# Performance work log

Hardware: AMD Instinct MI355X
Metric: run time of the kernel (lower is better)

Reference implementation:

```python
import jax, jax.numpy as jnp
import numpy as np

R_MAX = 32
S_MAX = 2
C_Z = 128
NTB = 2 * R_MAX + 2 + 1  # num_tok_pos_bins = 67
IN_DIM = 2 * NTB + (2 * S_MAX + 2) + 1  # 141


def _compute_bins(asym_id, entity_id, residue_index, token_index, sym_id, mask):
    # Pairwise [B, N, N] bucket indices, matching the torch module exactly.
    same_chain = asym_id[..., :, None] == asym_id[..., None, :]
    same_entity = entity_id[..., :, None] == entity_id[..., None, :]
    d_res = jnp.where(
        same_chain,
        jnp.clip(residue_index[..., :, None] - residue_index[..., None, :] + R_MAX, 0, 2 * R_MAX),
        2 * R_MAX + 1,
    )
    same_res = residue_index[..., :, None] == residue_index[..., None, :]
    tok_dist = token_index[..., :, None] - token_index[..., None, :] + R_MAX
    d_tok = jnp.where(same_chain & same_res, jnp.clip(tok_dist, 0, 2 * R_MAX), 2 * R_MAX + 1)
    d_chain = jnp.where(
        same_entity,
        jnp.clip(sym_id[..., :, None] - sym_id[..., None, :] + S_MAX, 0, 2 * S_MAX),
        2 * S_MAX + 1,
    )
    # index-removal spoofing: masked pairs go to the last token-position bin
    d_tok = jnp.where(mask, NTB - 1, d_tok)
    d_res = jnp.where(mask, NTB - 1, d_res)
    return d_res, d_tok, same_entity, d_chain


def setup_inputs() -> dict:
    key = jax.random.key(0)
    ks = jax.random.split(key, 7)
    B, N = 1, 768
    asym_id = jax.random.randint(ks[0], (B, N), 0, 4, dtype=jnp.int32)
    entity_id = jax.random.randint(ks[1], (B, N), 0, 3, dtype=jnp.int32)
    residue_index = jnp.sort(jax.random.randint(ks[2], (B, N), 0, 200, dtype=jnp.int32), axis=-1)
    token_index = jnp.sort(jax.random.randint(ks[3], (B, N), 0, 300, dtype=jnp.int32), axis=-1)
    sym_id = jax.random.randint(ks[4], (B, N), 0, 4, dtype=jnp.int32)
    unindexing_pair_mask = jax.random.randint(ks[5], (B, N, N), 0, 2) > 0
    W = jax.random.normal(ks[6], (IN_DIM, C_Z), dtype=jnp.float32) * 0.02
    return {
        "asym_id": asym_id,
        "entity_id": entity_id,
        "residue_index": residue_index,
        "token_index": token_index,
        "sym_id": sym_id,
        "unindexing_pair_mask": unindexing_pair_mask,
        "W": W,
    }


def reference(asym_id, entity_id, residue_index, token_index, sym_id, unindexing_pair_mask, W):
    d_res, d_tok, same_entity, d_chain = _compute_bins(
        asym_id, entity_id, residue_index, token_index, sym_id, unindexing_pair_mask
    )
    # linear(one_hot concat) == gather-sum of weight row blocks (same math, fused):
    # concat layout: [relpos (NTB) | reltoken (NTB) | same_entity (1) | relchain (2*S_MAX+2)]
    W_res = W[:NTB]                      # [67, c_z]
    W_tok = W[NTB:2 * NTB]               # [67, c_z]
    w_ent = W[2 * NTB]                   # [c_z]
    W_chain = W[2 * NTB + 1:]            # [6, c_z]
    out = (
        W_res[d_res]
        + W_tok[d_tok]
        + same_entity.astype(W.dtype)[..., None] * w_ent
        + W_chain[d_chain]
    )  # [B, N, N, c_z]
    return out
```

## Files before the change

kernel.cpp:

```cpp
#include <hip/hip_runtime.h>

#define R_MAX 32
#define S_MAX 2
#define C_Z   128
#define NTB   (2 * R_MAX + 2 + 1)
#define IN_DIM (2 * NTB + (2 * S_MAX + 2) + 1)

__device__ __forceinline__ int clampi(int x, int lo, int hi) {
    return min(max(x, lo), hi);
}

__global__ __launch_bounds__(256) void relpos_kernel(
    const int* __restrict__ asym_id,
    const int* __restrict__ entity_id,
    const int* __restrict__ residue_index,
    const int* __restrict__ token_index,
    const int* __restrict__ sym_id,
    const int* __restrict__ mask,
    const float* __restrict__ W,
    float* __restrict__ out,
    int N, long long total_pairs)
{
    long long t = (long long)blockIdx.x * blockDim.x + threadIdx.x;
    int chunk = (int)(t & 31);
    long long p = t >> 5;
    if (p >= total_pairs) return;

    long long row_i = p / N;
    int j_local = (int)(p - row_i * (long long)N);
    long long b = row_i / N;
    long long row_j = b * (long long)N + j_local;

    int ai = asym_id[row_i],        aj = asym_id[row_j];
    int ei = entity_id[row_i],      ej = entity_id[row_j];
    int ri = residue_index[row_i],  rj = residue_index[row_j];
    int ti = token_index[row_i],    tj = token_index[row_j];
    int si = sym_id[row_i],         sj = sym_id[row_j];

    bool same_chain  = (ai == aj);
    bool same_entity = (ei == ej);
    bool same_res    = (ri == rj);

    int d_res   = same_chain ? clampi(ri - rj + R_MAX, 0, 2 * R_MAX) : (2 * R_MAX + 1);
    int d_tok   = (same_chain && same_res) ? clampi(ti - tj + R_MAX, 0, 2 * R_MAX)
                                           : (2 * R_MAX + 1);
    int d_chain = same_entity ? clampi(si - sj + S_MAX, 0, 2 * S_MAX) : (2 * S_MAX + 1);

    if (mask[p] != 0) { d_tok = NTB - 1; d_res = NTB - 1; }

    const float4* Wr = (const float4*)(W + (size_t)d_res * C_Z);
    const float4* Wt = (const float4*)(W + (size_t)(NTB + d_tok) * C_Z);
    const float4* We = (const float4*)(W + (size_t)(2 * NTB) * C_Z);
    const float4* Wc = (const float4*)(W + (size_t)(2 * NTB + 1 + d_chain) * C_Z);

    float4 r  = Wr[chunk];
    float4 tk = Wt[chunk];
    float4 e  = We[chunk];
    float4 c  = Wc[chunk];

    float se = same_entity ? 1.0f : 0.0f;
    float4 o;
    o.x = r.x + tk.x + se * e.x + c.x;
    o.y = r.y + tk.y + se * e.y + c.y;
    o.z = r.z + tk.z + se * e.z + c.z;
    o.w = r.w + tk.w + se * e.w + c.w;

    ((float4*)out)[p * 32 + chunk] = o;
}

extern "C" void kernel_launch(void* const* d_in, const int* in_sizes, int n_in,
                              void* d_out, int out_size, void* d_ws, size_t ws_size,
                              hipStream_t stream) {
    const int*   asym_id       = (const int*)d_in[0];
    const int*   entity_id     = (const int*)d_in[1];
    const int*   residue_index = (const int*)d_in[2];
    const int*   token_index   = (const int*)d_in[3];
    const int*   sym_id        = (const int*)d_in[4];
    const int*   mask          = (const int*)d_in[5];
    const float* W             = (const float*)d_in[6];
    float*       out           = (float*)d_out;

    long long BN      = in_sizes[0];
    long long mask_sz = in_sizes[5];
    int N = (int)(mask_sz / BN);
    long long total_pairs = mask_sz;
    long long total_threads = total_pairs * 32;

    const int block = 256;
    unsigned grid = (unsigned)((total_threads + block - 1) / block);

    relpos_kernel<<<grid, block, 0, stream>>>(
        asym_id, entity_id, residue_index, token_index, sym_id,
        mask, W, out, N, total_pairs);
}
```

Before: 363.3 us.

## Compute pair bin codes once per pair in shared memory, then gather rows

Restructures the launch into a 2D grid of (row, 256-column tile). Each thread first computes one pair's bucket indices and packs them into a single int in shared memory. Then 8 pairs are processed per iteration, with 32 lanes per pair writing float4 chunks of the output row. This removes the redundant per-chunk recomputation of indices, mask loads and 64-bit divisions that the old one-thread-per-float4 layout did. It adds a __syncthreads and a loop with fewer, larger blocks, which may reduce latency hiding on what is a store-bandwidth-bound kernel.

```diff
diff --git a/kernel.cpp b/kernel.cpp
--- a/kernel.cpp
+++ b/kernel.cpp
@@ -5,6 +5,7 @@
 #define C_Z   128
 #define NTB   (2 * R_MAX + 2 + 1)
 #define IN_DIM (2 * NTB + (2 * S_MAX + 2) + 1)
+#define JT   256
 
 __device__ __forceinline__ int clampi(int x, int lo, int hi) {
     return min(max(x, lo), hi);
@@ -19,53 +20,81 @@
     const int* __restrict__ mask,
     const float* __restrict__ W,
     float* __restrict__ out,
-    int N, long long total_pairs)
+    int N)
 {
-    long long t = (long long)blockIdx.x * blockDim.x + threadIdx.x;
-    int chunk = (int)(t & 31);
-    long long p = t >> 5;
-    if (p >= total_pairs) return;
+    __shared__ int code_s[JT];
 
-    long long row_i = p / N;
-    int j_local = (int)(p - row_i * (long long)N);
-    long long b = row_i / N;
-    long long row_j = b * (long long)N + j_local;
+    const int tid = threadIdx.x;
+    const int row = blockIdx.y;
+    const int jb  = blockIdx.x * JT;
+    const int b   = row / N;
 
-    int ai = asym_id[row_i],        aj = asym_id[row_j];
-    int ei = entity_id[row_i],      ej = entity_id[row_j];
-    int ri = residue_index[row_i],  rj = residue_index[row_j];
-    int ti = token_index[row_i],    tj = token_index[row_j];
-    int si = sym_id[row_i],         sj = sym_id[row_j];
+    const int ai = asym_id[row];
+    const int ei = entity_id[row];
+    const int ri = residue_index[row];
+    const int ti = token_index[row];
+    const int si = sym_id[row];
 
-    bool same_chain  = (ai == aj);
-    bool same_entity = (ei == ej);
-    bool same_res    = (ri == rj);
+    {
+        int j = jb + tid;
+        int code = 0;
+        if (j < N) {
+            int jrow = b * N + j;
+            int aj = asym_id[jrow];
+            int ej = entity_id[jrow];
+            int rj = residue_index[jrow];
+            int tj = token_index[jrow];
+            int sj = sym_id[jrow];
 
-    int d_res   = same_chain ? clampi(ri - rj + R_MAX, 0, 2 * R_MAX) : (2 * R_MAX + 1);
-    int d_tok   = (same_chain && same_res) ? clampi(ti - tj + R_MAX, 0, 2 * R_MAX)
-                                           : (2 * R_MAX + 1);
-    int d_chain = same_entity ? clampi(si - sj + S_MAX, 0, 2 * S_MAX) : (2 * S_MAX + 1);
+            bool same_chain  = (ai == aj);
+            bool same_entity = (ei == ej);
+            bool same_res    = (ri == rj);
 
-    if (mask[p] != 0) { d_tok = NTB - 1; d_res = NTB - 1; }
+            int d_res   = same_chain ? clampi(ri - rj + R_MAX, 0, 2 * R_MAX) : (2 * R_MAX + 1);
+            int d_tok   = (same_chain && same_res) ? clampi(ti - tj + R_MAX, 0, 2 * R_MAX)
+                                                   : (2 * R_MAX + 1);
+            int d_chain = same_entity ? clampi(si - sj + S_MAX, 0, 2 * S_MAX) : (2 * S_MAX + 1);
 
-    const float4* Wr = (const float4*)(W + (size_t)d_res * C_Z);
-    const float4* Wt = (const float4*)(W + (size_t)(NTB + d_tok) * C_Z);
-    const float4* We = (const float4*)(W + (size_t)(2 * NTB) * C_Z);
-    const float4* Wc = (const float4*)(W + (size_t)(2 * NTB + 1 + d_chain) * C_Z);
+            if (mask[(long long)row * N + j] != 0) { d_res = NTB - 1; d_tok = NTB - 1; }
 
-    float4 r  = Wr[chunk];
-    float4 tk = Wt[chunk];
-    float4 e  = We[chunk];
-    float4 c  = Wc[chunk];
+            code = d_res | (d_tok << 7) | (d_chain << 14) | (same_entity ? (1 << 17) : 0);
+        }
+        code_s[tid] = code;
+    }
+    __syncthreads();
 
-    float se = same_entity ? 1.0f : 0.0f;
-    float4 o;
-    o.x = r.x + tk.x + se * e.x + c.x;
-    o.y = r.y + tk.y + se * e.y + c.y;
-    o.z = r.z + tk.z + se * e.z + c.z;
-    o.w = r.w + tk.w + se * e.w + c.w;
+    const int chunk = tid & 31;
+    const int psub  = tid >> 5;
+    const float4* __restrict__ W4 = (const float4*)W;
 
-    ((float4*)out)[p * 32 + chunk] = o;
+    const float4 e = W4[(2 * NTB) * 32 + chunk];
+
+    float4* __restrict__ outp = (float4*)out + ((long long)row * N + jb) * 32;
+    const int jmax = min(JT, N - jb);
+
+    #pragma unroll 4
+    for (int it = 0; it < JT / 8; ++it) {
+        int pair = it * 8 + psub;
+        if (pair >= jmax) break;
+        int code = code_s[pair];
+
+        int d_res   = code & 127;
+        int d_tok   = (code >> 7) & 127;
+        int d_chain = (code >> 14) & 7;
+        float se    = (code >> 17) ? 1.0f : 0.0f;
+
+        float4 r = W4[d_res * 32 + chunk];
+        float4 t = W4[(NTB + d_tok) * 32 + chunk];
+        float4 c = W4[(2 * NTB + 1 + d_chain) * 32 + chunk];
+
+        float4 o;
+        o.x = r.x + t.x + se * e.x + c.x;
+        o.y = r.y + t.y + se * e.y + c.y;
+        o.z = r.z + t.z + se * e.z + c.z;
+        o.w = r.w + t.w + se * e.w + c.w;
+
+        outp[(long long)pair * 32 + chunk] = o;
+    }
 }
 
 extern "C" void kernel_launch(void* const* d_in, const int* in_sizes, int n_in,
@@ -83,13 +112,11 @@
     long long BN      = in_sizes[0];
     long long mask_sz = in_sizes[5];
     int N = (int)(mask_sz / BN);
-    long long total_pairs = mask_sz;
-    long long total_threads = total_pairs * 32;
 
-    const int block = 256;
-    unsigned grid = (unsigned)((total_threads + block - 1) / block);
+    dim3 grid((unsigned)((N + JT - 1) / JT), (unsigned)BN);
+    dim3 block(256);
 
     relpos_kernel<<<grid, block, 0, stream>>>(
         asym_id, entity_id, residue_index, token_index, sym_id,
-        mask, W, out, N, total_pairs);
+        mask, W, out, N);
 }
```

New measurement: 361.4 us. No clear change (-0.5%).
